# Kernel optimization log

Measured on AMD Instinct MI355X. Metric: run time of the kernel, lower is better.

Reference implementation:

```python
import jax, jax.numpy as jnp
import numpy as np

NUM_EMBEDDINGS = 1024
EMBEDDING_DIM = 256

def setup_inputs() -> dict:
    key = jax.random.key(0)
    k1, k2 = jax.random.split(key)
    z_e = jax.random.normal(k1, (32, 256, 64, 64), dtype=jnp.float32)
    # nn.Embedding weight init uniform_(-1/K, 1/K)
    lim = 1.0 / NUM_EMBEDDINGS
    codebook = jax.random.uniform(k2, (NUM_EMBEDDINGS, EMBEDDING_DIM), dtype=jnp.float32,
                                  minval=-lim, maxval=lim)
    return {"z_e": z_e, "codebook": codebook}

def reference(z_e, codebook):
    B, C, H, W = z_e.shape
    # [B,C,H,W] -> [B*H*W, C]
    z_flat = jnp.transpose(z_e, (0, 2, 3, 1)).reshape(-1, C)
    # squared L2 distances: ||z||^2 + ||e||^2 - 2 z.e  -> [N, K]
    distances = (jnp.sum(z_flat ** 2, axis=1, keepdims=True)
                 + jnp.sum(codebook ** 2, axis=1)
                 - 2.0 * jnp.matmul(z_flat, codebook.T))
    encoding_indices = jnp.argmin(distances, axis=1)  # [N]
    z_q = codebook[encoding_indices].reshape(B, H, W, C)
    z_q = jnp.transpose(z_q, (0, 3, 1, 2))  # [B,C,H,W]
    sg = jax.lax.stop_gradient
    codebook_loss = jnp.mean((sg(z_q) - z_e) ** 2)
    commitment_loss = jnp.mean((sg(z_e) - z_q) ** 2)
    return z_q, codebook_loss + 0.25 * commitment_loss, encoding_indices
```

## Files before the change

### kernel.cpp

```cpp
#include <hip/hip_runtime.h>
#include <stdint.h>

typedef __attribute__((ext_vector_type(8))) _Float16 half8;
typedef __attribute__((ext_vector_type(4))) float f32x4;

#define CDIM 256
#define KCODES 1024
#define NPTS 131072
#define ZQ_ELEMS 33554432u
#define CAP 32768
#define MARGIN 3.0e-4f

#define WS_IMG 0
#define WS_S2 (16 * 65536)
#define WS_IDX (WS_S2 + 4096)
#define WS_PART (WS_IDX + NPTS * 4)
#define WS_CNT (WS_PART + 65536)
#define WS_LIST (WS_CNT + 64)

__device__ __forceinline__ float np_pairwise_sq_256(const float* x) {
    float res[2];
#pragma unroll
    for (int h = 0; h < 2; h++) {
        const float* a = x + h * 128;
        float r[8];
#pragma unroll
        for (int j = 0; j < 8; j++) r[j] = __fmul_rn(a[j], a[j]);
#pragma unroll
        for (int i = 8; i < 128; i += 8)
#pragma unroll
            for (int j = 0; j < 8; j++)
                r[j] = __fadd_rn(r[j], __fmul_rn(a[i + j], a[i + j]));
        res[h] = __fadd_rn(__fadd_rn(__fadd_rn(r[0], r[1]), __fadd_rn(r[2], r[3])),
                           __fadd_rn(__fadd_rn(r[4], r[5]), __fadd_rn(r[6], r[7])));
    }
    return __fadd_rn(res[0], res[1]);
}

__global__ __launch_bounds__(256) void vq_prep(const float* __restrict__ cb,
                                               unsigned char* __restrict__ img,
                                               int* __restrict__ cnt) {
    int t = threadIdx.x;
    if (blockIdx.x == 0 && t == 0) *cnt = 0;
    int codeLocal = t >> 5;
    int cg = t & 31;
    int k = blockIdx.x * 8 + codeLocal;
    const float* row = cb + k * CDIM + cg * 8;
    union H { _Float16 h[8]; uint4 u; } hi;
#pragma unroll
    for (int j = 0; j < 8; j++) hi.h[j] = (_Float16)(row[j] * 1024.f);
    int chunk = k >> 5, rowi = k & 31;
    int ks = cg >> 2, l4 = cg & 3;
    int q = rowi >> 4, l15 = rowi & 15;
    int lane = l4 * 16 + l15;
    *(uint4*)(img + chunk * 16384 + ((ks * 2 + q) << 10) + lane * 16) = hi.u;
}

__global__ __launch_bounds__(256) void vq_s2prep(const float* __restrict__ cb,
                                                 float* __restrict__ s2) {
    __shared__ float rows[32 * 261];
    int t = threadIdx.x;
    int k0 = blockIdx.x * 32;
#pragma unroll
    for (int i = 0; i < 8; i++) {
        int u = i * 256 + t;
        int row = u >> 6, c4 = u & 63;
        float4 v = *(const float4*)&cb[(size_t)(k0 + row) * CDIM + c4 * 4];
        float* d = &rows[row * 261 + c4 * 4];
        d[0] = v.x; d[1] = v.y; d[2] = v.z; d[3] = v.w;
    }
    __syncthreads();
    if (t < 32) s2[k0 + t] = np_pairwise_sq_256(&rows[t * 261]);
}

__global__ __launch_bounds__(256, 2) void vq_dist(const float* __restrict__ z,
                                                  const unsigned char* __restrict__ img,
                                                  const float* __restrict__ s2g,
                                                  int* __restrict__ outIdx,
                                                  int* __restrict__ cnt,
                                                  int* __restrict__ list,
                                                  float* __restrict__ partial) {
    __shared__ __align__(16) unsigned char smem[3][16384];
    __shared__ float e2s[1024];
    __shared__ float lred[4];
    int t = threadIdx.x;
    int lane = t & 63, wave = t >> 6;
    int l15 = lane & 15, l4 = lane >> 4;
    int blk0 = blockIdx.x * 256;
    int wbase = blk0 + wave * 64;
    int b = blk0 >> 12;
    int hwb0 = blk0 & 4095;
    const float* zb = z + (size_t)b * (CDIM * 4096);
    unsigned char* sbase = &smem[0][0];

#pragma unroll
    for (int i = 0; i < 4; i++) e2s[t + i * 256] = s2g[t + i * 256];

    half8 aHi[4][8];
    float s1p[4] = {0.f, 0.f, 0.f, 0.f};
#pragma unroll
    for (int ks = 0; ks < 8; ks++) {
        __syncthreads();
#pragma unroll
        for (int i = 0; i < 8; i++) {
            int u = i * 256 + t;
            int row = u >> 6, col16 = u & 63;
            const float* gsrc = zb + (size_t)(ks * 32 + row) * 4096 + hwb0 + col16 * 4;
            __builtin_amdgcn_global_load_lds(
                (const __attribute__((address_space(1))) void*)gsrc,
                (__attribute__((address_space(3))) void*)(sbase + (size_t)u * 16), 16, 0, 0);
        }
        __syncthreads();
#pragma unroll
        for (int m = 0; m < 4; m++) {
            half8 h;
            float ss = s1p[m];
#pragma unroll
            for (int j = 0; j < 8; j++) {
                float f = *(const float*)(sbase +
                        (size_t)(((l4 * 8 + j) << 8) + wave * 64 + m * 16 + l15) * 4) * 32.f;
                h[j] = (_Float16)f;
                ss = fmaf(f, f, ss);
            }
            aHi[m][ks] = h;
            s1p[m] = ss;
        }
    }
    __syncthreads();
#pragma unroll
    for (int m = 0; m < 4; m++) {
        s1p[m] += __shfl_xor(s1p[m], 16);
        s1p[m] += __shfl_xor(s1p[m], 32);
    }

#pragma unroll
    for (int i = 0; i < 4; i++) {
        size_t off = (size_t)(i * 256 + t) * 16;
        __builtin_amdgcn_global_load_lds(
            (const __attribute__((address_space(1))) void*)(img + off),
            (__attribute__((address_space(3))) void*)(&smem[0][0] + off), 16, 0, 0);
    }
#pragma unroll
    for (int i = 0; i < 4; i++) {
        size_t off = (size_t)(i * 256 + t) * 16;
        __builtin_amdgcn_global_load_lds(
            (const __attribute__((address_space(1))) void*)(img + 16384 + off),
            (__attribute__((address_space(3))) void*)(&smem[1][0] + off), 16, 0, 0);
    }

    float bestv[4][4], bestv2[4][4];
    int besti[4][4];
#pragma unroll
    for (int m = 0; m < 4; m++)
#pragma unroll
        for (int j = 0; j < 4; j++) { bestv[m][j] = 3.0e38f; bestv2[m][j] = 3.0e38f; besti[m][j] = 0; }

    int i0 = 0, i1 = 1, i2 = 2;
    for (int chunk = 0; chunk < 32; chunk++) {
        if (chunk < 31) asm volatile("s_waitcnt vmcnt(4)" ::: "memory");
        else            asm volatile("s_waitcnt vmcnt(0)" ::: "memory");
        __builtin_amdgcn_s_barrier();

        if (chunk + 2 < 32) {
            const unsigned char* src = img + (size_t)(chunk + 2) * 16384;
            unsigned char* dst = &smem[0][0] + (size_t)i2 * 16384;
#pragma unroll
            for (int i = 0; i < 4; i++) {
                size_t off = (size_t)(i * 256 + t) * 16;
                __builtin_amdgcn_global_load_lds(
                    (const __attribute__((address_space(1))) void*)(src + off),
                    (__attribute__((address_space(3))) void*)(dst + off), 16, 0, 0);
            }
        }

        f32x4 acc[4][2];
#pragma unroll
        for (int m = 0; m < 4; m++)
#pragma unroll
            for (int q = 0; q < 2; q++) acc[m][q] = (f32x4){0.f, 0.f, 0.f, 0.f};

        const unsigned char* bufc = &smem[0][0] + (size_t)i0 * 16384 + lane * 16;
#pragma unroll
        for (int ks = 0; ks < 8; ks++) {
            half8 b0 = *(const half8*)(bufc + (ks << 11));
            half8 b1 = *(const half8*)(bufc + (ks << 11) + 1024);
#pragma unroll
            for (int m = 0; m < 4; m++) {
                acc[m][0] = __builtin_amdgcn_mfma_f32_16x16x32_f16(aHi[m][ks], b0, acc[m][0], 0, 0, 0);
                acc[m][1] = __builtin_amdgcn_mfma_f32_16x16x32_f16(aHi[m][ks], b1, acc[m][1], 0, 0, 0);
            }
        }
#pragma unroll
        for (int q = 0; q < 2; q++) {
            int code = chunk * 32 + q * 16 + l15;
            float ev = e2s[code];
#pragma unroll
            for (int m = 0; m < 4; m++)
#pragma unroll
                for (int j = 0; j < 4; j++) {
                    float s = fmaf(acc[m][q][j], -6.103515625e-05f, ev);
                    if (s < bestv[m][j]) { bestv2[m][j] = bestv[m][j]; bestv[m][j] = s; besti[m][j] = code; }
                    else if (s < bestv2[m][j]) bestv2[m][j] = s;
                }
        }
        int tmp = i0; i0 = i1; i1 = i2; i2 = tmp;
    }

    float lsum = 0.f;
#pragma unroll
    for (int m = 0; m < 4; m++)
#pragma unroll
        for (int j = 0; j < 4; j++) {
            float v = bestv[m][j], v2 = bestv2[m][j];
            int idx = besti[m][j];
#pragma unroll
            for (int off = 1; off < 16; off <<= 1) {
                float ov = __shfl_xor(v, off);
                float ov2 = __shfl_xor(v2, off);
                int oi = __shfl_xor(idx, off);
                if (ov < v || (ov == v && oi < idx)) { v2 = fminf(v, ov2); v = ov; idx = oi; }
                else v2 = fminf(v2, ov);
            }
            int r = l4 * 4 + j;
            float S1r = __shfl(s1p[m], r) * 9.765625e-4f;
            if (l15 == 0) {
                lsum += S1r + v;
                int p = wbase + m * 16 + l4 * 4 + j;
                outIdx[p] = idx;
                if (v2 - v < MARGIN) {
                    int pos = atomicAdd(cnt, 1);
                    if (pos < CAP) list[pos] = p;
                }
            }
        }
#pragma unroll
    for (int off = 32; off > 0; off >>= 1) lsum += __shfl_down(lsum, off);
    if (lane == 0) lred[wave] = lsum;
    __syncthreads();
    if (t == 0) partial[blockIdx.x] = lred[0] + lred[1] + lred[2] + lred[3];
}

__global__ __launch_bounds__(256) void vq_cbt(const float* __restrict__ cb,
                                              float* __restrict__ cbT) {
    int k = blockIdx.x * 256 + threadIdx.x;
    for (int c = 0; c < 256; c++) cbT[c * 1024 + k] = cb[(size_t)k * 256 + c];
}

__global__ __launch_bounds__(256) void vq_rescue(const float* __restrict__ z,
                                                 const float* __restrict__ cbT,
                                                 const float* __restrict__ s2,
                                                 const int* __restrict__ list,
                                                 const int* __restrict__ cnt,
                                                 int* __restrict__ outIdx) {
    __shared__ float zs[8][256];
    __shared__ float S1s[8];
    __shared__ float rv[256];
    __shared__ int ri[256];
    int n = *cnt; if (n > CAP) n = CAP;
    int t = threadIdx.x;
    for (int base = blockIdx.x * 8; base < n; base += gridDim.x * 8) {
        int npts = n - base; if (npts > 8) npts = 8;
        __syncthreads();
        {
            int pp = t >> 5, c0 = (t & 31) * 8;
            if (pp < npts) {
                int p = list[base + pp];
                int b = p >> 12, hw = p & 4095;
                const float* zp = z + ((size_t)b << 20) + hw;
#pragma unroll
                for (int j = 0; j < 8; j++) zs[pp][c0 + j] = zp[(size_t)(c0 + j) << 12];
            }
        }
        __syncthreads();
        if (t < npts) S1s[t] = np_pairwise_sq_256(zs[t]);
        __syncthreads();

        float d[8][4];
#pragma unroll
        for (int pp = 0; pp < 8; pp++)
#pragma unroll
            for (int q = 0; q < 4; q++) d[pp][q] = 0.f;
        for (int c = 0; c < 256; c++) {
            const float* er = cbT + c * 1024 + t;
            float e0 = er[0], e1 = er[256], e2v = er[512], e3 = er[768];
#pragma unroll
            for (int pp = 0; pp < 8; pp++) {
                float zc = zs[pp][c];
                d[pp][0] = fmaf(zc, e0, d[pp][0]);
                d[pp][1] = fmaf(zc, e1, d[pp][1]);
                d[pp][2] = fmaf(zc, e2v, d[pp][2]);
                d[pp][3] = fmaf(zc, e3, d[pp][3]);
            }
        }
        float s2v[4] = {s2[t], s2[256 + t], s2[512 + t], s2[768 + t]};

        float bv[8]; int bi[8];
#pragma unroll
        for (int pp = 0; pp < 8; pp++) {
            float v = 3.4e38f; int i0 = 0;
#pragma unroll
            for (int q = 0; q < 4; q++) {
                float dist = __fsub_rn(__fadd_rn(S1s[pp], s2v[q]), __fmul_rn(2.0f, d[pp][q]));
                if (dist < v) { v = dist; i0 = q * 256 + t; }
            }
            bv[pp] = v; bi[pp] = i0;
        }
        for (int pp = 0; pp < 8; pp++) {
            if (pp >= npts) break;
            rv[t] = bv[pp]; ri[t] = bi[pp];
            __syncthreads();
            for (int sft = 128; sft > 0; sft >>= 1) {
                if (t < sft) {
                    if (rv[t + sft] < rv[t] || (rv[t + sft] == rv[t] && ri[t + sft] < ri[t])) {
                        rv[t] = rv[t + sft]; ri[t] = ri[t + sft];
                    }
                }
                __syncthreads();
            }
            if (t == 0) outIdx[list[base + pp]] = ri[0];
            __syncthreads();
        }
    }
}

__global__ __launch_bounds__(256) void vq_gather(const float* __restrict__ cb,
                                                 const int* __restrict__ idxs,
                                                 float* __restrict__ out) {
    int unit = blockIdx.x * 256 + threadIdx.x;
    int hw4 = unit & 1023;
    int cgb = unit >> 10;
    int b = cgb >> 5, cg = cgb & 31;

    int4 ids = *(const int4*)&idxs[(b << 12) + hw4 * 4];
    float va[4][8];
#pragma unroll
    for (int e = 0; e < 4; e++) {
        int id = (e == 0) ? ids.x : (e == 1) ? ids.y : (e == 2) ? ids.z : ids.w;
        const float4* cr = (const float4*)(cb + (size_t)id * CDIM + cg * 8);
        float4 v0 = cr[0], v1 = cr[1];
        va[e][0] = v0.x; va[e][1] = v0.y; va[e][2] = v0.z; va[e][3] = v0.w;
        va[e][4] = v1.x; va[e][5] = v1.y; va[e][6] = v1.z; va[e][7] = v1.w;
    }
#pragma unroll
    for (int j = 0; j < 8; j++) {
        size_t addr = (((size_t)(b * 256 + cg * 8 + j)) << 12) + hw4 * 4;
        float4 ov = {va[0][j], va[1][j], va[2][j], va[3][j]};
        *(float4*)&out[addr] = ov;
    }
    if (cg == 0) {
        size_t ib = (size_t)ZQ_ELEMS + 1u + (b << 12) + hw4 * 4;
        out[ib + 0] = (float)ids.x;
        out[ib + 1] = (float)ids.y;
        out[ib + 2] = (float)ids.z;
        out[ib + 3] = (float)ids.w;
    }
}

__global__ __launch_bounds__(512) void vq_finalize(const float* __restrict__ partial,
                                                   float* __restrict__ out) {
    int t = threadIdx.x;
    double s = (t < 512) ? (double)partial[t] : 0.0;
#pragma unroll
    for (int off = 32; off > 0; off >>= 1) s += __shfl_down(s, off);
    __shared__ double sd[8];
    if ((t & 63) == 0) sd[t >> 6] = s;
    __syncthreads();
    if (t == 0) {
        double tot = sd[0] + sd[1] + sd[2] + sd[3] + sd[4] + sd[5] + sd[6] + sd[7];
        out[ZQ_ELEMS] = (float)(1.25 * tot / (double)ZQ_ELEMS);
    }
}

extern "C" void kernel_launch(void* const* d_in, const int* in_sizes, int n_in,
                              void* d_out, int out_size, void* d_ws, size_t ws_size,
                              hipStream_t stream) {
    const float* z = (const float*)d_in[0];
    const float* cb = (const float*)d_in[1];
    unsigned char* ws = (unsigned char*)d_ws;
    unsigned char* img = ws + WS_IMG;
    float* cbT = (float*)(ws + WS_IMG);
    float* s2 = (float*)(ws + WS_S2);
    int* idx = (int*)(ws + WS_IDX);
    float* partial = (float*)(ws + WS_PART);
    int* cnt = (int*)(ws + WS_CNT);
    int* list = (int*)(ws + WS_LIST);
    float* out = (float*)d_out;

    vq_prep<<<128, 256, 0, stream>>>(cb, img, cnt);
    vq_s2prep<<<32, 256, 0, stream>>>(cb, s2);
    vq_dist<<<512, 256, 0, stream>>>(z, img, s2, idx, cnt, list, partial);
    vq_cbt<<<4, 256, 0, stream>>>(cb, cbT);
    vq_rescue<<<512, 256, 0, stream>>>(z, cbT, s2, list, cnt, idx);
    vq_gather<<<4096, 256, 0, stream>>>(cb, idx, out);
    vq_finalize<<<1, 512, 0, stream>>>(partial, out);
}
```

Before: 335.1 us.

## Halve per-block point tile, read codebook straight from global, merge prep kernels

The distance kernel now covers 128 points per block instead of 256 and launches twice as many blocks with a higher occupancy hint. It drops the triple-buffered LDS staging of the fp16 codebook image and loads B fragments directly from global/L2 each chunk. The two codebook prep kernels are fused into one launch, and finalize grows to 1024 threads to cover the doubled partial sums. This trades codebook reuse across points per block (more L2 traffic) for fewer registers, less LDS, higher occupancy and one fewer launch.

```diff
diff --git a/kernel.cpp b/kernel.cpp
--- a/kernel.cpp
+++ b/kernel.cpp
@@ -37,30 +37,14 @@
     return __fadd_rn(res[0], res[1]);
 }
 
-__global__ __launch_bounds__(256) void vq_prep(const float* __restrict__ cb,
-                                               unsigned char* __restrict__ img,
-                                               int* __restrict__ cnt) {
-    int t = threadIdx.x;
-    if (blockIdx.x == 0 && t == 0) *cnt = 0;
-    int codeLocal = t >> 5;
-    int cg = t & 31;
-    int k = blockIdx.x * 8 + codeLocal;
-    const float* row = cb + k * CDIM + cg * 8;
-    union H { _Float16 h[8]; uint4 u; } hi;
-#pragma unroll
-    for (int j = 0; j < 8; j++) hi.h[j] = (_Float16)(row[j] * 1024.f);
-    int chunk = k >> 5, rowi = k & 31;
-    int ks = cg >> 2, l4 = cg & 3;
-    int q = rowi >> 4, l15 = rowi & 15;
-    int lane = l4 * 16 + l15;
-    *(uint4*)(img + chunk * 16384 + ((ks * 2 + q) << 10) + lane * 16) = hi.u;
-}
-
-__global__ __launch_bounds__(256) void vq_s2prep(const float* __restrict__ cb,
-                                                 float* __restrict__ s2) {
+__global__ __launch_bounds__(256) void vq_prepall(const float* __restrict__ cb,
+                                                  unsigned char* __restrict__ img,
+                                                  float* __restrict__ s2,
+                                                  int* __restrict__ cnt) {
     __shared__ float rows[32 * 261];
     int t = threadIdx.x;
     int k0 = blockIdx.x * 32;
+    if (blockIdx.x == 0 && t == 0) *cnt = 0;
 #pragma unroll
     for (int i = 0; i < 8; i++) {
         int u = i * 256 + t;
@@ -71,54 +55,65 @@
     }
     __syncthreads();
     if (t < 32) s2[k0 + t] = np_pairwise_sq_256(&rows[t * 261]);
-}
-
-__global__ __launch_bounds__(256, 2) void vq_dist(const float* __restrict__ z,
+#pragma unroll
+    for (int i = 0; i < 4; i++) {
+        int u = i * 256 + t;
+        int cl = u >> 5, cg = u & 31;
+        union H { _Float16 h[8]; uint4 u4; } hv;
+#pragma unroll
+        for (int j = 0; j < 8; j++) hv.h[j] = (_Float16)(rows[cl * 261 + cg * 8 + j] * 1024.f);
+        int ks = cg >> 2, l4 = cg & 3;
+        int q = cl >> 4, l15 = cl & 15;
+        int lane = l4 * 16 + l15;
+        *(uint4*)(img + (size_t)blockIdx.x * 16384 + ((ks * 2 + q) << 10) + lane * 16) = hv.u4;
+    }
+}
+
+__global__ __launch_bounds__(256, 4) void vq_dist(const float* __restrict__ z,
                                                   const unsigned char* __restrict__ img,
                                                   const float* __restrict__ s2g,
                                                   int* __restrict__ outIdx,
                                                   int* __restrict__ cnt,
                                                   int* __restrict__ list,
                                                   float* __restrict__ partial) {
-    __shared__ __align__(16) unsigned char smem[3][16384];
+    __shared__ __align__(16) unsigned char az[16384];
     __shared__ float e2s[1024];
     __shared__ float lred[4];
     int t = threadIdx.x;
     int lane = t & 63, wave = t >> 6;
     int l15 = lane & 15, l4 = lane >> 4;
-    int blk0 = blockIdx.x * 256;
-    int wbase = blk0 + wave * 64;
+    int blk0 = blockIdx.x * 128;
+    int wbase = blk0 + wave * 32;
     int b = blk0 >> 12;
     int hwb0 = blk0 & 4095;
     const float* zb = z + (size_t)b * (CDIM * 4096);
-    unsigned char* sbase = &smem[0][0];
 
 #pragma unroll
     for (int i = 0; i < 4; i++) e2s[t + i * 256] = s2g[t + i * 256];
 
-    half8 aHi[4][8];
-    float s1p[4] = {0.f, 0.f, 0.f, 0.f};
+    half8 aHi[2][8];
+    float s1p[2] = {0.f, 0.f};
 #pragma unroll
     for (int ks = 0; ks < 8; ks++) {
         __syncthreads();
 #pragma unroll
-        for (int i = 0; i < 8; i++) {
+        for (int i = 0; i < 4; i++) {
             int u = i * 256 + t;
-            int row = u >> 6, col16 = u & 63;
-            const float* gsrc = zb + (size_t)(ks * 32 + row) * 4096 + hwb0 + col16 * 4;
+            int row = u >> 5, col4 = u & 31;
+            const float* gsrc = zb + (size_t)(ks * 32 + row) * 4096 + hwb0 + col4 * 4;
             __builtin_amdgcn_global_load_lds(
                 (const __attribute__((address_space(1))) void*)gsrc,
-                (__attribute__((address_space(3))) void*)(sbase + (size_t)u * 16), 16, 0, 0);
-        }
-        __syncthreads();
-#pragma unroll
-        for (int m = 0; m < 4; m++) {
+                (__attribute__((address_space(3))) void*)(az + (size_t)u * 16), 16, 0, 0);
+        }
+        __syncthreads();
+#pragma unroll
+        for (int m = 0; m < 2; m++) {
             half8 h;
             float ss = s1p[m];
 #pragma unroll
             for (int j = 0; j < 8; j++) {
-                float f = *(const float*)(sbase +
-                        (size_t)(((l4 * 8 + j) << 8) + wave * 64 + m * 16 + l15) * 4) * 32.f;
+                float f = *(const float*)(az +
+                        (size_t)(((l4 * 8 + j) * 128) + wave * 32 + m * 16 + l15) * 4) * 32.f;
                 h[j] = (_Float16)f;
                 ss = fmaf(f, f, ss);
             }
@@ -128,64 +123,32 @@
     }
     __syncthreads();
 #pragma unroll
-    for (int m = 0; m < 4; m++) {
+    for (int m = 0; m < 2; m++) {
         s1p[m] += __shfl_xor(s1p[m], 16);
         s1p[m] += __shfl_xor(s1p[m], 32);
     }
 
-#pragma unroll
-    for (int i = 0; i < 4; i++) {
-        size_t off = (size_t)(i * 256 + t) * 16;
-        __builtin_amdgcn_global_load_lds(
-            (const __attribute__((address_space(1))) void*)(img + off),
-            (__attribute__((address_space(3))) void*)(&smem[0][0] + off), 16, 0, 0);
-    }
-#pragma unroll
-    for (int i = 0; i < 4; i++) {
-        size_t off = (size_t)(i * 256 + t) * 16;
-        __builtin_amdgcn_global_load_lds(
-            (const __attribute__((address_space(1))) void*)(img + 16384 + off),
-            (__attribute__((address_space(3))) void*)(&smem[1][0] + off), 16, 0, 0);
-    }
-
-    float bestv[4][4], bestv2[4][4];
-    int besti[4][4];
-#pragma unroll
-    for (int m = 0; m < 4; m++)
+    float bestv[2][4], bestv2[2][4];
+    int besti[2][4];
+#pragma unroll
+    for (int m = 0; m < 2; m++)
 #pragma unroll
         for (int j = 0; j < 4; j++) { bestv[m][j] = 3.0e38f; bestv2[m][j] = 3.0e38f; besti[m][j] = 0; }
 
-    int i0 = 0, i1 = 1, i2 = 2;
+    const unsigned char* ib = img + (size_t)lane * 16;
     for (int chunk = 0; chunk < 32; chunk++) {
-        if (chunk < 31) asm volatile("s_waitcnt vmcnt(4)" ::: "memory");
-        else            asm volatile("s_waitcnt vmcnt(0)" ::: "memory");
-        __builtin_amdgcn_s_barrier();
-
-        if (chunk + 2 < 32) {
-            const unsigned char* src = img + (size_t)(chunk + 2) * 16384;
-            unsigned char* dst = &smem[0][0] + (size_t)i2 * 16384;
-#pragma unroll
-            for (int i = 0; i < 4; i++) {
-                size_t off = (size_t)(i * 256 + t) * 16;
-                __builtin_amdgcn_global_load_lds(
-                    (const __attribute__((address_space(1))) void*)(src + off),
-                    (__attribute__((address_space(3))) void*)(dst + off), 16, 0, 0);
-            }
-        }
-
-        f32x4 acc[4][2];
-#pragma unroll
-        for (int m = 0; m < 4; m++)
+        const unsigned char* cb8 = ib + (size_t)chunk * 16384;
+        f32x4 acc[2][2];
+#pragma unroll
+        for (int m = 0; m < 2; m++)
 #pragma unroll
             for (int q = 0; q < 2; q++) acc[m][q] = (f32x4){0.f, 0.f, 0.f, 0.f};
-
-        const unsigned char* bufc = &smem[0][0] + (size_t)i0 * 16384 + lane * 16;
 #pragma unroll
         for (int ks = 0; ks < 8; ks++) {
-            half8 b0 = *(const half8*)(bufc + (ks << 11));
-            half8 b1 = *(const half8*)(bufc + (ks << 11) + 1024);
-#pragma unroll
-            for (int m = 0; m < 4; m++) {
+            half8 b0 = *(const half8*)(cb8 + (ks << 11));
+            half8 b1 = *(const half8*)(cb8 + (ks << 11) + 1024);
+#pragma unroll
+            for (int m = 0; m < 2; m++) {
                 acc[m][0] = __builtin_amdgcn_mfma_f32_16x16x32_f16(aHi[m][ks], b0, acc[m][0], 0, 0, 0);
                 acc[m][1] = __builtin_amdgcn_mfma_f32_16x16x32_f16(aHi[m][ks], b1, acc[m][1], 0, 0, 0);
             }
@@ -195,7 +158,7 @@
             int code = chunk * 32 + q * 16 + l15;
             float ev = e2s[code];
 #pragma unroll
-            for (int m = 0; m < 4; m++)
+            for (int m = 0; m < 2; m++)
 #pragma unroll
                 for (int j = 0; j < 4; j++) {
                     float s = fmaf(acc[m][q][j], -6.103515625e-05f, ev);
@@ -203,12 +166,11 @@
                     else if (s < bestv2[m][j]) bestv2[m][j] = s;
                 }
         }
-        int tmp = i0; i0 = i1; i1 = i2; i2 = tmp;
     }
 
     float lsum = 0.f;
 #pragma unroll
-    for (int m = 0; m < 4; m++)
+    for (int m = 0; m < 2; m++)
 #pragma unroll
         for (int j = 0; j < 4; j++) {
             float v = bestv[m][j], v2 = bestv2[m][j];
@@ -356,17 +318,18 @@
     }
 }
 
-__global__ __launch_bounds__(512) void vq_finalize(const float* __restrict__ partial,
-                                                   float* __restrict__ out) {
+__global__ __launch_bounds__(1024) void vq_finalize(const float* __restrict__ partial,
+                                                    float* __restrict__ out) {
     int t = threadIdx.x;
-    double s = (t < 512) ? (double)partial[t] : 0.0;
+    double s = (double)partial[t];
 #pragma unroll
     for (int off = 32; off > 0; off >>= 1) s += __shfl_down(s, off);
-    __shared__ double sd[8];
+    __shared__ double sd[16];
     if ((t & 63) == 0) sd[t >> 6] = s;
     __syncthreads();
     if (t == 0) {
-        double tot = sd[0] + sd[1] + sd[2] + sd[3] + sd[4] + sd[5] + sd[6] + sd[7];
+        double tot = 0.0;
+        for (int i = 0; i < 16; i++) tot += sd[i];
         out[ZQ_ELEMS] = (float)(1.25 * tot / (double)ZQ_ELEMS);
     }
 }
@@ -386,11 +349,10 @@
     int* list = (int*)(ws + WS_LIST);
     float* out = (float*)d_out;
 
-    vq_prep<<<128, 256, 0, stream>>>(cb, img, cnt);
-    vq_s2prep<<<32, 256, 0, stream>>>(cb, s2);
-    vq_dist<<<512, 256, 0, stream>>>(z, img, s2, idx, cnt, list, partial);
+    vq_prepall<<<32, 256, 0, stream>>>(cb, img, s2, cnt);
+    vq_dist<<<1024, 256, 0, stream>>>(z, img, s2, idx, cnt, list, partial);
     vq_cbt<<<4, 256, 0, stream>>>(cb, cbT);
     vq_rescue<<<512, 256, 0, stream>>>(z, cbT, s2, list, cnt, idx);
     vq_gather<<<4096, 256, 0, stream>>>(cb, idx, out);
-    vq_finalize<<<1, 512, 0, stream>>>(partial, out);
-}
+    vq_finalize<<<1, 1024, 0, stream>>>(partial, out);
+}
```

Result: slower. 351.0 us (+4.7%).
